# Performance work log

Measured on AMD Instinct MI355X. Metric: run time of the kernel, lower is better.

The kernel has to match this reference:

```python
import jax, jax.numpy as jnp
import numpy as np

H = 8          # head_count
C = 512        # emb_dim
DH = C // H    # head_emb_size = 64
FF = 4 * C     # feed_forward hidden = 2048
EPS = 1e-5     # nn.LayerNorm default eps


def setup_inputs() -> dict:
    key = jax.random.key(0)
    ks = jax.random.split(key, 16)
    s = lambda fan_in: 1.0 / np.sqrt(fan_in)
    inp = {
        "x": jax.random.normal(ks[0], (4, 2048, C), dtype=jnp.float32),
        "ln1_g": jnp.ones((C,), jnp.float32),
        "ln1_b": jnp.zeros((C,), jnp.float32),
        # per-head QKV projections, stacked over heads: [H, C, DH]
        "Wq": jax.random.uniform(ks[1], (H, C, DH), jnp.float32, -s(C), s(C)),
        "bq": jax.random.uniform(ks[2], (H, DH), jnp.float32, -s(C), s(C)),
        "Wk": jax.random.uniform(ks[3], (H, C, DH), jnp.float32, -s(C), s(C)),
        "bk": jax.random.uniform(ks[4], (H, DH), jnp.float32, -s(C), s(C)),
        "Wv": jax.random.uniform(ks[5], (H, C, DH), jnp.float32, -s(C), s(C)),
        "bv": jax.random.uniform(ks[6], (H, DH), jnp.float32, -s(C), s(C)),
        "Wp": jax.random.uniform(ks[7], (C, C), jnp.float32, -s(C), s(C)),
        "bp": jax.random.uniform(ks[8], (C,), jnp.float32, -s(C), s(C)),
        "ln2_g": jnp.ones((C,), jnp.float32),
        "ln2_b": jnp.zeros((C,), jnp.float32),
        "W1": jax.random.uniform(ks[9], (C, FF), jnp.float32, -s(C), s(C)),
        "b1": jax.random.uniform(ks[10], (FF,), jnp.float32, -s(C), s(C)),
        "W2": jax.random.uniform(ks[11], (FF, C), jnp.float32, -s(FF), s(FF)),
        "b2": jax.random.uniform(ks[12], (C,), jnp.float32, -s(FF), s(FF)),
    }
    return inp


def _layernorm(x, g, b):
    mu = jnp.mean(x, axis=-1, keepdims=True)
    var = jnp.mean((x - mu) ** 2, axis=-1, keepdims=True)
    return (x - mu) * jax.lax.rsqrt(var + EPS) * g + b


def _block(x, ln1_g, ln1_b, Wq, bq, Wk, bk, Wv, bv, Wp, bp, ln2_g, ln2_b, W1, b1, W2, b2):
    B, T, _ = x.shape
    h = _layernorm(x, ln1_g, ln1_b)
    # per-head projections, vectorized over heads: [B,H,T,DH]
    Q = jnp.einsum("btc,hcd->bhtd", h, Wq) + bq[None, :, None, :]
    K = jnp.einsum("btc,hcd->bhtd", h, Wk) + bk[None, :, None, :]
    V = jnp.einsum("btc,hcd->bhtd", h, Wv) + bv[None, :, None, :]
    wei = jnp.einsum("bhtd,bhsd->bhts", Q, K) / jnp.sqrt(jnp.float32(DH))
    causal = jnp.tril(jnp.ones((T, T), dtype=bool))
    wei = jnp.where(causal, wei, jnp.float32(-1e9))  # masked_fill(-1e9)
    wei = jax.nn.softmax(wei, axis=-1)
    out = jnp.einsum("bhts,bhsd->bhtd", wei, V)      # [B,H,T,DH]
    # concat heads (head order = ModuleList order) -> [B,T,C]
    out = out.transpose(0, 2, 1, 3).reshape(B, T, H * DH)
    attn = out @ Wp + bp
    x = x + attn
    h2 = _layernorm(x, ln2_g, ln2_b)
    ff = jax.nn.relu(h2 @ W1 + b1) @ W2 + b2
    return x + ff


def reference(x, ln1_g, ln1_b, Wq, bq, Wk, bk, Wv, bv, Wp, bp, ln2_g, ln2_b, W1, b1, W2, b2):
    return _block(x, ln1_g, ln1_b, Wq, bq, Wk, bk, Wv, bv, Wp, bp, ln2_g, ln2_b, W1, b1, W2, b2)
```

## Files before the change

### kernel.cpp

```cpp
#include <hip/hip_runtime.h>

typedef unsigned short u16;
typedef unsigned int   u32;
typedef __attribute__((ext_vector_type(4))) int   i32x4;
typedef __attribute__((ext_vector_type(4))) float f32x4;
typedef __attribute__((ext_vector_type(4))) unsigned short u16x4;
typedef __attribute__((ext_vector_type(8))) unsigned short u16x8;

#define DEVI static __device__ __forceinline__

DEVI u16 f2b(float f) {
  u32 u = __builtin_bit_cast(u32, f);
  return (u16)((u + 0x7FFFu + ((u >> 16) & 1u)) >> 16);
}

DEVI void mfma16(f32x4& d, i32x4 a, i32x4 b) {
  asm("v_mfma_f32_16x16x32_bf16 %0, %1, %2, %0" : "+v"(d) : "v"(a), "v"(b));
}

DEVI void gload16(const void* g, void* l) {
  __builtin_amdgcn_global_load_lds(
      (const __attribute__((address_space(1))) void*)g,
      (__attribute__((address_space(3))) void*)l, 16, 0, 0);
}

DEVI int swz(int row, int b) {
  return (row << 7) + (((b >> 4) ^ (row & 7)) << 4) + (b & 15);
}

__global__ __launch_bounds__(256) void pack_qkv_w(
    const float* __restrict__ Wq, const float* __restrict__ Wk,
    const float* __restrict__ Wv, u16* __restrict__ dst)
{
  int idx = blockIdx.x * 256 + threadIdx.x;
  int n = idx >> 9, c = idx & 511;
  const float* W = (n < 512) ? Wq : (n < 1024) ? Wk : Wv;
  int nn = n & 511;
  int h = nn >> 6, d = nn & 63;
  dst[idx] = f2b(W[(size_t)((h << 9) + c) * 64 + d]);
}

__global__ __launch_bounds__(256) void trans_bf16(
    const float* __restrict__ src, u16* __restrict__ dst, int srbits, int SC)
{
  int idx = blockIdx.x * 256 + threadIdx.x;
  if (idx >= (SC << srbits)) return;
  int a = idx >> srbits;
  int b = idx & ((1 << srbits) - 1);
  dst[idx] = f2b(src[(size_t)b * SC + a]);
}

__global__ __launch_bounds__(256) void ln_kernel(
    const float* __restrict__ x, const float* __restrict__ gamma,
    const float* __restrict__ beta, u16* __restrict__ out)
{
  const int lane = threadIdx.x & 63;
  const int row = blockIdx.x * 4 + (threadIdx.x >> 6);
  const float4* xr = (const float4*)(x + (size_t)row * 512) + lane * 2;
  float4 a0 = xr[0], a1 = xr[1];
  float s  = a0.x + a0.y + a0.z + a0.w + a1.x + a1.y + a1.z + a1.w;
  float sq = a0.x*a0.x + a0.y*a0.y + a0.z*a0.z + a0.w*a0.w
           + a1.x*a1.x + a1.y*a1.y + a1.z*a1.z + a1.w*a1.w;
  #pragma unroll
  for (int o = 32; o > 0; o >>= 1) { s += __shfl_xor(s, o); sq += __shfl_xor(sq, o); }
  const float mu = s * (1.0f / 512.0f);
  const float rstd = rsqrtf(sq * (1.0f / 512.0f) - mu * mu + 1e-5f);
  const float4* g4 = (const float4*)gamma + lane * 2;
  const float4* b4 = (const float4*)beta  + lane * 2;
  float4 g0 = g4[0], g1 = g4[1], b0 = b4[0], b1 = b4[1];
  float xv[8] = {a0.x,a0.y,a0.z,a0.w,a1.x,a1.y,a1.z,a1.w};
  float gv[8] = {g0.x,g0.y,g0.z,g0.w,g1.x,g1.y,g1.z,g1.w};
  float bv[8] = {b0.x,b0.y,b0.z,b0.w,b1.x,b1.y,b1.z,b1.w};
  u16x8 ov;
  #pragma unroll
  for (int j = 0; j < 8; j++) ov[j] = f2b((xv[j] - mu) * rstd * gv[j] + bv[j]);
  *(u16x8*)(out + (size_t)row * 512 + lane * 8) = ov;
}

template<int KD, int EPI>
__global__ __launch_bounds__(256) void gemm_bt(
    const u16* __restrict__ A, const u16* __restrict__ Bt,
    const float* __restrict__ bias0, const float* __restrict__ bias1,
    const float* __restrict__ bias2, const float* __restrict__ resid,
    void* __restrict__ out0, void* __restrict__ out1, void* __restrict__ out2)
{
  __shared__ __align__(16) u16 sA[128 * 32];
  __shared__ __align__(16) u16 sB[128 * 32];
  const int tid = threadIdx.x, lane = tid & 63, w = tid >> 6;
  const int m0 = blockIdx.x * 128, n0 = blockIdx.y * 128;
  const int wr = w >> 1, wc = w & 1, r = lane & 15, gq = lane >> 4;

  f32x4 acc[4][4] = {};

  const int o0 = w * 2048 + lane * 16;
  const int row0 = o0 >> 6, kb0 = o0 & 63;
  const int o1 = o0 + 1024;
  const int row1 = o1 >> 6, kb1 = o1 & 63;
  const char* Ab = (const char*)A;
  const char* Bb = (const char*)Bt;
  char* sAd = (char*)sA + w * 2048;
  char* sBd = (char*)sB + w * 2048;

  for (int k0 = 0; k0 < KD; k0 += 32) {
    const int kbyte = k0 * 2;
    gload16(Ab + (size_t)(m0 + row0) * (KD * 2) + kbyte + kb0, sAd);
    gload16(Ab + (size_t)(m0 + row1) * (KD * 2) + kbyte + kb1, sAd + 1024);
    gload16(Bb + (size_t)(n0 + row0) * (KD * 2) + kbyte + kb0, sBd);
    gload16(Bb + (size_t)(n0 + row1) * (KD * 2) + kbyte + kb1, sBd + 1024);
    __syncthreads();
    i32x4 af[4], bfr[4];
    #pragma unroll
    for (int i = 0; i < 4; i++)
      af[i] = *(const i32x4*)(sA + (wr * 64 + i * 16 + r) * 32 + gq * 8);
    #pragma unroll
    for (int j = 0; j < 4; j++)
      bfr[j] = *(const i32x4*)(sB + (wc * 64 + j * 16 + r) * 32 + gq * 8);
    #pragma unroll
    for (int i = 0; i < 4; i++)
      #pragma unroll
      for (int j = 0; j < 4; j++)
        mfma16(acc[i][j], af[i], bfr[j]);
    __syncthreads();
  }

  #pragma unroll
  for (int i = 0; i < 4; i++) {
    #pragma unroll
    for (int j = 0; j < 4; j++) {
      const int mb = m0 + wr * 64 + i * 16 + gq * 4;
      const int nc = n0 + wc * 64 + j * 16 + r;
      #pragma unroll
      for (int e = 0; e < 4; e++) {
        const int m = mb + e;
        float v = acc[i][j][e];
        if (EPI == 0) {
          float bias; u16* dst;
          if (nc < 512)       { bias = bias0[nc];        dst = (u16*)out0; }
          else if (nc < 1024) { bias = bias1[nc - 512];  dst = (u16*)out1; }
          else                { bias = bias2[nc - 1024]; dst = (u16*)out2; }
          v += bias;
          const int nn = nc & 511, h = nn >> 6, d = nn & 63;
          const int bb = m >> 11, t = m & 2047;
          dst[(size_t)((bb * 8 + h) * 2048 + t) * 64 + d] = f2b(v);
        } else if (EPI == 1) {
          v += bias0[nc] + resid[(size_t)m * 512 + nc];
          ((float*)out0)[(size_t)m * 512 + nc] = v;
        } else {
          v += bias0[nc];
          v = fmaxf(v, 0.0f);
          ((u16*)out0)[(size_t)m * 2048 + nc] = f2b(v);
        }
      }
    }
  }
}

__global__ __launch_bounds__(256) void attn_kernel(
    const u16* __restrict__ Q, const u16* __restrict__ K,
    const u16* __restrict__ V, u16* __restrict__ O)
{
  __shared__ __align__(16) char lds[40960];
  const int tid = threadIdx.x, lane = tid & 63, w = tid >> 6;
  const int p = blockIdx.x & 15, bh = blockIdx.x >> 4;
  const int r = lane & 15, gq = lane >> 4;
  const u16* Qb = Q + (size_t)bh * (2048 * 64);
  const u16* Kb = K + (size_t)bh * (2048 * 64);
  const u16* Vb = V + (size_t)bh * (2048 * 64);
  const int bb = bh >> 3, hh = bh & 7;
  char* Pb = lds + 32768 + w * 2048;

  const int sv = (tid & 15) * 4;
  const int dv = (tid >> 4) * 4;
  u16x4 vr[4];

#define STAGEK(s0g, buf) do {                                              \
    _Pragma("unroll")                                                      \
    for (int i_ = 0; i_ < 2; i_++) {                                       \
      int o_ = w * 2048 + i_ * 1024 + lane * 16;                           \
      int so_ = o_ ^ (((o_ >> 7) & 7) << 4);                               \
      gload16((const char*)(Kb + (size_t)(s0g) * 64) + so_,                \
              lds + (buf) * 8192 + w * 2048 + i_ * 1024);                  \
    } } while (0)

#define LOADV(s0g) do {                                                    \
    _Pragma("unroll")                                                      \
    for (int j_ = 0; j_ < 4; j_++)                                         \
      vr[j_] = *(const u16x4*)(Vb + (size_t)((s0g) + sv + j_) * 64 + dv);  \
    } while (0)

#define WRITEV(buf) do {                                                   \
    _Pragma("unroll")                                                      \
    for (int dd_ = 0; dd_ < 4; dd_++) {                                    \
      u16x4 val_ = {vr[0][dd_], vr[1][dd_], vr[2][dd_], vr[3][dd_]};       \
      *(u16x4*)(lds + 16384 + (buf) * 8192 + swz(dv + dd_, sv * 2)) = val_;\
    } } while (0)

  #pragma unroll 1
  for (int half = 0; half < 2; half++) {
    const int qt = half ? p : (31 - p);
    const int q0 = qt << 6;
    const int qg = q0 + w * 16 + r;

    i32x4 qf[2];
    qf[0] = *(const i32x4*)(Qb + (size_t)(q0 + w * 16 + r) * 64 + gq * 8);
    qf[1] = *(const i32x4*)(Qb + (size_t)(q0 + w * 16 + r) * 64 + 32 + gq * 8);

    STAGEK(0, 0);
    LOADV(0);
    WRITEV(0);
    __syncthreads();

    f32x4 accO[4] = {};
    float m_run = -1e30f, l_run = 0.0f;

    for (int t = 0; t <= qt; t++) {
      const int cb = t & 1, nb = cb ^ 1;
      const bool diag = (t == qt);
      const int s0 = t << 6;
      if (!diag) {
        STAGEK(s0 + 64, nb);
        LOADV(s0 + 64);
      }

      f32x4 st[4] = {};
      const int sbmax = diag ? (w + 1) : 4;
      #pragma unroll
      for (int kd = 0; kd < 2; kd++)
        #pragma unroll
        for (int sb = 0; sb < 4; sb++)
          if (sb < sbmax) {
            i32x4 kf = *(const i32x4*)(lds + cb * 8192 + swz(sb * 16 + r, kd * 64 + gq * 16));
            mfma16(st[sb], kf, qf[kd]);
          }

      float tmax = -1e30f;
      if (diag) {
        #pragma unroll
        for (int sb = 0; sb < 4; sb++)
          #pragma unroll
          for (int e = 0; e < 4; e++) {
            int sg = s0 + sb * 16 + gq * 4 + e;
            float v = st[sb][e] * 0.125f;
            v = (sg <= qg) ? v : -1e30f;
            st[sb][e] = v;
            tmax = fmaxf(tmax, v);
          }
      } else {
        #pragma unroll
        for (int sb = 0; sb < 4; sb++)
          #pragma unroll
          for (int e = 0; e < 4; e++) {
            float v = st[sb][e] * 0.125f;
            st[sb][e] = v;
            tmax = fmaxf(tmax, v);
          }
      }
      tmax = fmaxf(tmax, __shfl_xor(tmax, 16));
      tmax = fmaxf(tmax, __shfl_xor(tmax, 32));

      if (!__all(tmax <= m_run)) {
        const float mnew = fmaxf(m_run, tmax);
        const float alpha = __expf(m_run - mnew);
        l_run *= alpha;
        float ae[4];
        #pragma unroll
        for (int e = 0; e < 4; e++) ae[e] = __shfl(alpha, gq * 4 + e);
        #pragma unroll
        for (int db = 0; db < 4; db++)
          #pragma unroll
          for (int e = 0; e < 4; e++) accO[db][e] *= ae[e];
        m_run = mnew;
      }
      float rsum = 0.0f;
      #pragma unroll
      for (int sb = 0; sb < 4; sb++)
        #pragma unroll
        for (int e = 0; e < 4; e++) {
          float pv = __expf(st[sb][e] - m_run);
          st[sb][e] = pv;
          rsum += pv;
        }
      rsum += __shfl_xor(rsum, 16);
      rsum += __shfl_xor(rsum, 32);
      l_run += rsum;

      #pragma unroll
      for (int sb = 0; sb < 4; sb++) {
        u32 lo, hi;
        asm("v_cvt_pk_bf16_f32 %0, %1, %2" : "=v"(lo) : "v"(st[sb][0]), "v"(st[sb][1]));
        asm("v_cvt_pk_bf16_f32 %0, %1, %2" : "=v"(hi) : "v"(st[sb][2]), "v"(st[sb][3]));
        uint2 pk; pk.x = lo; pk.y = hi;
        *(uint2*)(Pb + swz(r, sb * 32 + gq * 8)) = pk;
      }

      const int kmax = diag ? ((w >> 1) + 1) : 2;
      #pragma unroll
      for (int ks = 0; ks < 2; ks++)
        if (ks < kmax) {
          i32x4 pf = *(const i32x4*)(Pb + swz(r, ks * 64 + gq * 16));
          #pragma unroll
          for (int db = 0; db < 4; db++) {
            i32x4 vf = *(const i32x4*)(lds + 16384 + cb * 8192 + swz(db * 16 + r, ks * 64 + gq * 16));
            mfma16(accO[db], pf, vf);
          }
        }

      if (!diag) WRITEV(nb);
      __syncthreads();
    }

    float le[4];
    #pragma unroll
    for (int e = 0; e < 4; e++) le[e] = 1.0f / __shfl(l_run, gq * 4 + e);
    #pragma unroll
    for (int db = 0; db < 4; db++)
      #pragma unroll
      for (int e = 0; e < 4; e++) {
        int qrow = q0 + w * 16 + gq * 4 + e;
        int d = db * 16 + r;
        O[(size_t)(bb * 2048 + qrow) * 512 + hh * 64 + d] = f2b(accO[db][e] * le[e]);
      }
  }
#undef STAGEK
#undef LOADV
#undef WRITEV
}

extern "C" void kernel_launch(void* const* d_in, const int* in_sizes, int n_in,
                              void* d_out, int out_size, void* d_ws, size_t ws_size,
                              hipStream_t stream)
{
  const float* x    = (const float*)d_in[0];
  const float* ln1g = (const float*)d_in[1];
  const float* ln1b = (const float*)d_in[2];
  const float* Wq   = (const float*)d_in[3];
  const float* bq   = (const float*)d_in[4];
  const float* Wk   = (const float*)d_in[5];
  const float* bk   = (const float*)d_in[6];
  const float* Wv   = (const float*)d_in[7];
  const float* bv   = (const float*)d_in[8];
  const float* Wp   = (const float*)d_in[9];
  const float* bp   = (const float*)d_in[10];
  const float* ln2g = (const float*)d_in[11];
  const float* ln2b = (const float*)d_in[12];
  const float* W1   = (const float*)d_in[13];
  const float* b1   = (const float*)d_in[14];
  const float* W2   = (const float*)d_in[15];
  const float* b2   = (const float*)d_in[16];

  char* ws = (char*)d_ws;
  const size_t MB = 1ull << 20;
  float* x1  = (float*)(ws);
  u16* hbuf  = (u16*)(ws + 16 * MB);
  u16* Qb    = (u16*)(ws + 24 * MB);
  u16* Kb    = (u16*)(ws + 32 * MB);
  u16* Vb    = (u16*)(ws + 40 * MB);
  u16* attn  = (u16*)(ws + 48 * MB);
  u16* fbuf  = (u16*)(ws + 24 * MB);
  u16* Wqkv  = (u16*)(ws + 56 * MB);
  u16* Wpt   = (u16*)(ws + 58 * MB);
  u16* W1t   = (u16*)(ws + 59 * MB);
  u16* W2t   = (u16*)(ws + 61 * MB);
  float* outf = (float*)d_out;

  pack_qkv_w<<<3072, 256, 0, stream>>>(Wq, Wk, Wv, Wqkv);
  trans_bf16<<<1024, 256, 0, stream>>>(Wp, Wpt, 9, 512);
  trans_bf16<<<4096, 256, 0, stream>>>(W1, W1t, 9, 2048);
  trans_bf16<<<4096, 256, 0, stream>>>(W2, W2t, 11, 512);
  ln_kernel<<<2048, 256, 0, stream>>>(x, ln1g, ln1b, hbuf);
  gemm_bt<512, 0><<<dim3(64, 12), 256, 0, stream>>>(hbuf, Wqkv, bq, bk, bv,
                                                    nullptr, Qb, Kb, Vb);
  attn_kernel<<<512, 256, 0, stream>>>(Qb, Kb, Vb, attn);
  gemm_bt<512, 1><<<dim3(64, 4), 256, 0, stream>>>(attn, Wpt, bp, nullptr, nullptr,
                                                   x, x1, nullptr, nullptr);
  ln_kernel<<<2048, 256, 0, stream>>>(x1, ln2g, ln2b, hbuf);
  gemm_bt<512, 2><<<dim3(64, 16), 256, 0, stream>>>(hbuf, W1t, b1, nullptr, nullptr,
                                                    nullptr, fbuf, nullptr, nullptr);
  gemm_bt<2048, 1><<<dim3(64, 4), 256, 0, stream>>>(fbuf, W2t, b2, nullptr, nullptr,
                                                    x1, outf, nullptr, nullptr);
}
```

Baseline: 183.4 us.

## Triple-buffer GEMM LDS loads and tile weight transposes through shared memory

The GEMM main loop now keeps three LDS stages and issues async global-to-LDS loads two k-steps ahead, waiting on partial vmcnt counts instead of draining every load per iteration. This is meant to hide global load latency behind MFMA work, at the cost of triple the LDS footprint, which may reduce occupancy. The weight conversion kernels are also replaced by 64x64 tiled transposes through LDS with coalesced vector reads and writes, replacing strided scalar accesses.

```diff
diff --git a/kernel.cpp b/kernel.cpp
--- a/kernel.cpp
+++ b/kernel.cpp
@@ -28,26 +28,60 @@
   return (row << 7) + (((b >> 4) ^ (row & 7)) << 4) + (b & 15);
 }
 
-__global__ __launch_bounds__(256) void pack_qkv_w(
+__global__ __launch_bounds__(256) void trans_tile(
+    const float* __restrict__ src, u16* __restrict__ dst, int R, int C)
+{
+  __shared__ u16 tile[64][72];
+  const int rb = blockIdx.x * 64, cb = blockIdx.y * 64;
+  const int t = threadIdx.x;
+  const int tr = t >> 2, tc = (t & 3) * 16;
+  const float* sp = src + (size_t)(rb + tr) * C + cb + tc;
+  #pragma unroll
+  for (int q = 0; q < 4; q++) {
+    float4 v = *(const float4*)(sp + q * 4);
+    tile[tr][tc + q*4 + 0] = f2b(v.x);
+    tile[tr][tc + q*4 + 1] = f2b(v.y);
+    tile[tr][tc + q*4 + 2] = f2b(v.z);
+    tile[tr][tc + q*4 + 3] = f2b(v.w);
+  }
+  __syncthreads();
+  const int dc = t >> 2, dr = (t & 3) * 16;
+  u16x8 o0, o1;
+  #pragma unroll
+  for (int j = 0; j < 8; j++) { o0[j] = tile[dr + j][dc]; o1[j] = tile[dr + 8 + j][dc]; }
+  u16* dp = dst + (size_t)(cb + dc) * R + rb + dr;
+  *(u16x8*)(dp) = o0;
+  *(u16x8*)(dp + 8) = o1;
+}
+
+__global__ __launch_bounds__(256) void pack_qkv_tile(
     const float* __restrict__ Wq, const float* __restrict__ Wk,
     const float* __restrict__ Wv, u16* __restrict__ dst)
 {
-  int idx = blockIdx.x * 256 + threadIdx.x;
-  int n = idx >> 9, c = idx & 511;
-  const float* W = (n < 512) ? Wq : (n < 1024) ? Wk : Wv;
-  int nn = n & 511;
-  int h = nn >> 6, d = nn & 63;
-  dst[idx] = f2b(W[(size_t)((h << 9) + c) * 64 + d]);
-}
-
-__global__ __launch_bounds__(256) void trans_bf16(
-    const float* __restrict__ src, u16* __restrict__ dst, int srbits, int SC)
-{
-  int idx = blockIdx.x * 256 + threadIdx.x;
-  if (idx >= (SC << srbits)) return;
-  int a = idx >> srbits;
-  int b = idx & ((1 << srbits) - 1);
-  dst[idx] = f2b(src[(size_t)b * SC + a]);
+  __shared__ u16 tile[64][72];
+  const int bid = blockIdx.x;
+  const int cb = (bid & 7) * 64, h = (bid >> 3) & 7, widx = bid >> 6;
+  const float* W = (widx == 0) ? Wq : (widx == 1) ? Wk : Wv;
+  const float* src = W + (size_t)h * 512 * 64;
+  const int t = threadIdx.x;
+  const int tr = t >> 2, tc = (t & 3) * 16;
+  const float* sp = src + (size_t)(cb + tr) * 64 + tc;
+  #pragma unroll
+  for (int q = 0; q < 4; q++) {
+    float4 v = *(const float4*)(sp + q * 4);
+    tile[tr][tc + q*4 + 0] = f2b(v.x);
+    tile[tr][tc + q*4 + 1] = f2b(v.y);
+    tile[tr][tc + q*4 + 2] = f2b(v.z);
+    tile[tr][tc + q*4 + 3] = f2b(v.w);
+  }
+  __syncthreads();
+  const int dc = t >> 2, dr = (t & 3) * 16;
+  u16x8 o0, o1;
+  #pragma unroll
+  for (int j = 0; j < 8; j++) { o0[j] = tile[dr + j][dc]; o1[j] = tile[dr + 8 + j][dc]; }
+  u16* dp = dst + (size_t)(widx * 512 + h * 64 + dc) * 512 + cb + dr;
+  *(u16x8*)(dp) = o0;
+  *(u16x8*)(dp + 8) = o1;
 }
 
 __global__ __launch_bounds__(256) void ln_kernel(
@@ -84,8 +118,9 @@
     const float* __restrict__ bias2, const float* __restrict__ resid,
     void* __restrict__ out0, void* __restrict__ out1, void* __restrict__ out2)
 {
-  __shared__ __align__(16) u16 sA[128 * 32];
-  __shared__ __align__(16) u16 sB[128 * 32];
+  __shared__ __align__(16) u16 sA[3][128 * 32];
+  __shared__ __align__(16) u16 sB[3][128 * 32];
+  constexpr int NSTEP = KD / 32;
   const int tid = threadIdx.x, lane = tid & 63, w = tid >> 6;
   const int m0 = blockIdx.x * 128, n0 = blockIdx.y * 128;
   const int wr = w >> 1, wc = w & 1, r = lane & 15, gq = lane >> 4;
@@ -98,30 +133,49 @@
   const int row1 = o1 >> 6, kb1 = o1 & 63;
   const char* Ab = (const char*)A;
   const char* Bb = (const char*)Bt;
-  char* sAd = (char*)sA + w * 2048;
-  char* sBd = (char*)sB + w * 2048;
-
-  for (int k0 = 0; k0 < KD; k0 += 32) {
-    const int kbyte = k0 * 2;
-    gload16(Ab + (size_t)(m0 + row0) * (KD * 2) + kbyte + kb0, sAd);
-    gload16(Ab + (size_t)(m0 + row1) * (KD * 2) + kbyte + kb1, sAd + 1024);
-    gload16(Bb + (size_t)(n0 + row0) * (KD * 2) + kbyte + kb0, sBd);
-    gload16(Bb + (size_t)(n0 + row1) * (KD * 2) + kbyte + kb1, sBd + 1024);
-    __syncthreads();
+
+#define STAGE(step, buf) do {                                                \
+    const int kbyte_ = (step) * 64;                                          \
+    char* sAd_ = (char*)sA + (buf) * 8192 + w * 2048;                        \
+    char* sBd_ = (char*)sB + (buf) * 8192 + w * 2048;                        \
+    gload16(Ab + (size_t)(m0 + row0) * (KD * 2) + kbyte_ + kb0, sAd_);       \
+    gload16(Ab + (size_t)(m0 + row1) * (KD * 2) + kbyte_ + kb1, sAd_ + 1024);\
+    gload16(Bb + (size_t)(n0 + row0) * (KD * 2) + kbyte_ + kb0, sBd_);       \
+    gload16(Bb + (size_t)(n0 + row1) * (KD * 2) + kbyte_ + kb1, sBd_ + 1024);\
+  } while (0)
+
+  STAGE(0, 0);
+  STAGE(1, 1);
+
+  for (int t = 0; t < NSTEP; t++) {
+    __builtin_amdgcn_sched_barrier(0);
+    __builtin_amdgcn_s_barrier();
+    if (t + 2 < NSTEP) {
+      STAGE(t + 2, (t + 2) % 3);
+      asm volatile("s_waitcnt vmcnt(8)" ::: "memory");
+    } else if (t + 1 < NSTEP) {
+      asm volatile("s_waitcnt vmcnt(4)" ::: "memory");
+    } else {
+      asm volatile("s_waitcnt vmcnt(0)" ::: "memory");
+    }
+    __builtin_amdgcn_sched_barrier(0);
+    __builtin_amdgcn_s_barrier();
+    const u16* sAc = sA[t % 3];
+    const u16* sBc = sB[t % 3];
     i32x4 af[4], bfr[4];
     #pragma unroll
     for (int i = 0; i < 4; i++)
-      af[i] = *(const i32x4*)(sA + (wr * 64 + i * 16 + r) * 32 + gq * 8);
+      af[i] = *(const i32x4*)(sAc + (wr * 64 + i * 16 + r) * 32 + gq * 8);
     #pragma unroll
     for (int j = 0; j < 4; j++)
-      bfr[j] = *(const i32x4*)(sB + (wc * 64 + j * 16 + r) * 32 + gq * 8);
+      bfr[j] = *(const i32x4*)(sBc + (wc * 64 + j * 16 + r) * 32 + gq * 8);
     #pragma unroll
     for (int i = 0; i < 4; i++)
       #pragma unroll
       for (int j = 0; j < 4; j++)
         mfma16(acc[i][j], af[i], bfr[j]);
-    __syncthreads();
   }
+#undef STAGE
 
   #pragma unroll
   for (int i = 0; i < 4; i++) {
@@ -140,8 +194,8 @@
           else                { bias = bias2[nc - 1024]; dst = (u16*)out2; }
           v += bias;
           const int nn = nc & 511, h = nn >> 6, d = nn & 63;
-          const int bb = m >> 11, t = m & 2047;
-          dst[(size_t)((bb * 8 + h) * 2048 + t) * 64 + d] = f2b(v);
+          const int bb = m >> 11, tt = m & 2047;
+          dst[(size_t)((bb * 8 + h) * 2048 + tt) * 64 + d] = f2b(v);
         } else if (EPI == 1) {
           v += bias0[nc] + resid[(size_t)m * 512 + nc];
           ((float*)out0)[(size_t)m * 512 + nc] = v;
@@ -363,10 +417,10 @@
   u16* W2t   = (u16*)(ws + 61 * MB);
   float* outf = (float*)d_out;
 
-  pack_qkv_w<<<3072, 256, 0, stream>>>(Wq, Wk, Wv, Wqkv);
-  trans_bf16<<<1024, 256, 0, stream>>>(Wp, Wpt, 9, 512);
-  trans_bf16<<<4096, 256, 0, stream>>>(W1, W1t, 9, 2048);
-  trans_bf16<<<4096, 256, 0, stream>>>(W2, W2t, 11, 512);
+  pack_qkv_tile<<<192, 256, 0, stream>>>(Wq, Wk, Wv, Wqkv);
+  trans_tile<<<dim3(8, 8),  256, 0, stream>>>(Wp, Wpt, 512, 512);
+  trans_tile<<<dim3(8, 32), 256, 0, stream>>>(W1, W1t, 512, 2048);
+  trans_tile<<<dim3(32, 8), 256, 0, stream>>>(W2, W2t, 2048, 512);
   ln_kernel<<<2048, 256, 0, stream>>>(x, ln1g, ln1b, hbuf);
   gemm_bt<512, 0><<<dim3(64, 12), 256, 0, stream>>>(hbuf, Wqkv, bq, bk, bv,
                                                     nullptr, Qb, Kb, Vb);
```

Result: faster. 177.6 us (-3.2%).
